# Kernel optimization log

Measured on AMD Instinct MI355X. Metric: run time of the kernel, lower is better.

The kernel has to match this reference:

```python
import jax, jax.numpy as jnp
import numpy as np

BETA = 0.25      # commitment loss weight
DECAY = 0.99     # EMA decay
EPS = 1e-5       # Laplace smoothing for counts


def setup_inputs() -> dict:
    key = jax.random.key(0)
    k1, k2, k3 = jax.random.split(key, 3)
    B, d, h, w, K = 16, 64, 64, 64, 1024
    z_e = jax.random.normal(k1, (B, d, h, w), dtype=jnp.float32)
    codebook = jax.random.normal(k2, (K, d), dtype=jnp.float32)
    ema_count = jnp.ones((K,), dtype=jnp.float32)
    ema_sum = jax.random.normal(k3, (K, d), dtype=jnp.float32)
    return {"z_e": z_e, "codebook": codebook, "ema_count": ema_count, "ema_sum": ema_sum}


def reference(z_e, codebook, ema_count, ema_sum):
    B, d, h, w = z_e.shape
    K = codebook.shape[0]
    # [B,d,h,w] -> [N,d], N = B*h*w
    z_flat = jnp.transpose(z_e, (0, 2, 3, 1)).reshape(-1, d)
    # squared euclidean distances [N,K]
    dist = (jnp.sum(z_flat * z_flat, axis=1, keepdims=True)
            - 2.0 * (z_flat @ codebook.T)
            + jnp.sum(codebook * codebook, axis=1)[None, :])
    indices = jnp.argmin(dist, axis=1)                      # [N] int
    e_k = codebook[indices].reshape(B, h, w, d).transpose(0, 3, 1, 2)  # [B,d,h,w]

    # --- EMA codebook update (training mode, no grad) ---
    zf = jax.lax.stop_gradient(z_flat)
    counts = jax.ops.segment_sum(jnp.ones((zf.shape[0],), dtype=zf.dtype), indices, num_segments=K)
    sums = jax.ops.segment_sum(zf, indices, num_segments=K)
    new_count = ema_count * DECAY + (1.0 - DECAY) * counts
    new_sum = ema_sum * DECAY + (1.0 - DECAY) * sums
    n = jnp.sum(new_count)
    count_s = (new_count + EPS) / (n + K * EPS) * n
    new_codebook = new_sum / count_s[:, None]

    # straight-through estimator
    e_k_ste = z_e + jax.lax.stop_gradient(e_k - z_e)
    L_commit = (jnp.mean((z_e - jax.lax.stop_gradient(e_k)) ** 2)
                + BETA * jnp.mean((jax.lax.stop_gradient(z_e) - e_k) ** 2))
    return (e_k_ste, indices.reshape(B, h, w), L_commit, new_codebook, new_count, new_sum)
```

## Files before the change

kernel.cpp:

```cpp
#include <hip/hip_runtime.h>
#include <hip/hip_bf16.h>
#include <hip/hip_fp16.h>

#define NB 16
#define DD 64
#define HW 4096
#define NTOT 65536
#define KC 1024

#define O_EK   0
#define O_IDX  4194304
#define O_L    4259840
#define O_CB   4259841
#define O_CNT  4325377
#define O_SUM  4326401

#define WS_IDX    0
#define WS_LCPART 65536
#define WS_N      66048
#define WS_CNORM  66560
#define WS_PSUM   67584
#define WS_PCNT   329728
#define WS_CBH    399360
#define WS_CBL    432128

typedef _Float16 v8h __attribute__((ext_vector_type(8)));
typedef float    v4f __attribute__((ext_vector_type(4)));
typedef unsigned short ush;

__global__ __launch_bounds__(256) void k_pre(const float* __restrict__ cb,
                                             const float* __restrict__ ema_count,
                                             float* __restrict__ cnorm,
                                             float* __restrict__ n_ws,
                                             unsigned short* __restrict__ cbh,
                                             unsigned short* __restrict__ cbl) {
    const int t = threadIdx.x;
    const int w = (blockIdx.x * 256 + t) >> 6;
    const int l = t & 63;
    float s = 0.f;
    if (l < 16) {
        float4 v = *(const float4*)(cb + (size_t)w * DD + l * 4);
        s = v.x * v.x + v.y * v.y + v.z * v.z + v.w * v.w;
    }
#pragma unroll
    for (int m = 1; m <= 8; m <<= 1) s += __shfl_xor(s, m, 64);
    if (l == 0) cnorm[w] = s;

    const int e4 = blockIdx.x * 256 + t;
    if (e4 < 16384) {
        float4 v4 = ((const float4*)cb)[e4];
        float sx = -2.f * v4.x, sy = -2.f * v4.y, sz = -2.f * v4.z, sw = -2.f * v4.w;
        __half hx = __float2half(sx), hy = __float2half(sy),
               hz = __float2half(sz), hw2 = __float2half(sw);
        ushort4 h4 = { __half_as_ushort(hx), __half_as_ushort(hy),
                       __half_as_ushort(hz), __half_as_ushort(hw2) };
        ((ushort4*)cbh)[e4] = h4;
        ushort4 l4 = { __half_as_ushort(__float2half(sx - __half2float(hx))),
                       __half_as_ushort(__float2half(sy - __half2float(hy))),
                       __half_as_ushort(__float2half(sz - __half2float(hz))),
                       __half_as_ushort(__float2half(sw - __half2float(hw2))) };
        ((ushort4*)cbl)[e4] = l4;
    }

    if (blockIdx.x == 0) {
        __shared__ float red[256];
        red[t] = ema_count[t] + ema_count[t + 256] + ema_count[t + 512] + ema_count[t + 768];
        __syncthreads();
        for (int s2 = 128; s2 >= 1; s2 >>= 1) {
            if (t < s2) red[t] += red[t + s2];
            __syncthreads();
        }
        if (t == 0) n_ws[0] = 0.99f * red[0] + 0.01f * 65536.0f;
    }
}

__global__ __launch_bounds__(512, 3) void k_argmin(const float* __restrict__ z_e,
                                                   const float* __restrict__ cbf,
                                                   const unsigned short* __restrict__ cbh,
                                                   const unsigned short* __restrict__ cbl,
                                                   const float* __restrict__ cnorm,
                                                   unsigned short* __restrict__ idx16,
                                                   float* __restrict__ out) {
    __shared__ __align__(16) unsigned char ldsAB[32768];
    __shared__ __align__(16) float slab[2048];
    __shared__ int idx_lds[128];
    __shared__ int flagrows[128];
    __shared__ int flagi1[128];
    __shared__ int flagi2[128];
    __shared__ int nflag;

    ush (*A2h)[128][8]  = (ush(*)[128][8])(ldsAB);
    ush (*A2l)[128][8]  = (ush(*)[128][8])(ldsAB + 16384);
    ush (*B2h)[8][64][8] = (ush(*)[8][64][8])(ldsAB);
    ush (*B2l)[8][64][8] = (ush(*)[8][64][8])(ldsAB + 16384);

    const int t  = threadIdx.x;
    const int n0 = blockIdx.x * 128;
    const int bb  = n0 >> 12;
    const int hw0 = n0 & 4095;
    const float* zbase = z_e + (size_t)bb * (DD * HW) + hw0;

    if (t == 0) nflag = 0;

    {
        const int jr   = t >> 5;
        const int m4   = (t & 31) << 2;
        const int chl  = t >> 8;
        const int cm   = t & 127;
        const int half = (t >> 7) & 1;
        for (int sl = 0; sl < 4; ++sl) {
            if (sl) __syncthreads();
            float4 v = *(const float4*)(zbase + (size_t)(sl * 16 + jr) * HW + m4);
            *(float4*)&slab[jr * 128 + m4] = v;
            __syncthreads();
            unsigned hv[2], lv[2];
#pragma unroll
            for (int p = 0; p < 2; ++p) {
                int jj = chl * 8 + half * 4 + p * 2;
                float v0 = slab[jj * 128 + cm];
                float v1 = slab[(jj + 1) * 128 + cm];
                __half h0 = __float2half(v0), h1 = __float2half(v1);
                __half l0 = __float2half(v0 - __half2float(h0));
                __half l1 = __float2half(v1 - __half2float(h1));
                hv[p] = (unsigned)__half_as_ushort(h0) | ((unsigned)__half_as_ushort(h1) << 16);
                lv[p] = (unsigned)__half_as_ushort(l0) | ((unsigned)__half_as_ushort(l1) << 16);
            }
            uint2 hq = {hv[0], hv[1]}, lq = {lv[0], lv[1]};
            *(uint2*)&A2h[sl * 2 + chl][cm][half * 4] = hq;
            *(uint2*)&A2l[sl * 2 + chl][cm][half * 4] = lq;
        }
    }
    __syncthreads();

    const int w    = t >> 6;
    const int lane = t & 63;
    const int c    = lane & 15;
    const int q    = lane >> 4;

    v8h Afh[2], Afl[2];
    {
        int m = 16 * w + c;
#pragma unroll
        for (int s = 0; s < 2; ++s) {
            Afh[s] = *(const v8h*)&A2h[s * 4 + q][m][0];
            Afl[s] = *(const v8h*)&A2l[s * 4 + q][m][0];
        }
    }
    __syncthreads();

    const int ch0   = t >> 6;
    const int code0 = t & 63;

    {
        size_t g0 = ((size_t)code0) * 64 + ch0 * 8;
        *(uint4*)&B2h[0][ch0][code0][0] = *(const uint4*)(cbh + g0);
        *(uint4*)&B2l[0][ch0][code0][0] = *(const uint4*)(cbl + g0);
    }
    __syncthreads();

    float m1f[4], m2f[4];
#pragma unroll
    for (int r = 0; r < 4; ++r) { m1f[r] = 3.4e38f; m2f[r] = 3.4e38f; }

    for (int kt = 0; kt < 16; ++kt) {
        const int cur = kt & 1, nxt = cur ^ 1;
        uint4 ph0, pl0;
        if (kt < 15) {
            size_t g0 = ((size_t)((kt + 1) * 64 + code0)) * 64 + ch0 * 8;
            ph0 = *(const uint4*)(cbh + g0);
            pl0 = *(const uint4*)(cbl + g0);
        }

#pragma unroll
        for (int sub = 0; sub < 4; ++sub) {
            const int cl = sub * 16 + c;
            v8h Bfh0 = *(const v8h*)&B2h[cur][q][cl][0];
            v8h Bfh1 = *(const v8h*)&B2h[cur][4 + q][cl][0];
            v8h Bfl0 = *(const v8h*)&B2l[cur][q][cl][0];
            v8h Bfl1 = *(const v8h*)&B2l[cur][4 + q][cl][0];
            const unsigned kg = (unsigned)(kt * 64 + cl);
            const float cnc = cnorm[kg];
            v4f acc = {cnc, cnc, cnc, cnc};
            acc = __builtin_amdgcn_mfma_f32_16x16x32_f16(Afh[0], Bfh0, acc, 0, 0, 0);
            acc = __builtin_amdgcn_mfma_f32_16x16x32_f16(Afh[1], Bfh1, acc, 0, 0, 0);
            acc = __builtin_amdgcn_mfma_f32_16x16x32_f16(Afh[0], Bfl0, acc, 0, 0, 0);
            acc = __builtin_amdgcn_mfma_f32_16x16x32_f16(Afh[1], Bfl1, acc, 0, 0, 0);
            acc = __builtin_amdgcn_mfma_f32_16x16x32_f16(Afl[0], Bfh0, acc, 0, 0, 0);
            acc = __builtin_amdgcn_mfma_f32_16x16x32_f16(Afl[1], Bfh1, acc, 0, 0, 0);
#pragma unroll
            for (int r = 0; r < 4; ++r) {
                unsigned vu = (__float_as_uint(acc[r]) & 0xFFFFFC00u) | kg;
                float vp = __uint_as_float(vu);
                m2f[r] = __builtin_amdgcn_fmed3f(m1f[r], m2f[r], vp);
                m1f[r] = fminf(m1f[r], vp);
            }
        }

        if (kt < 15) {
            *(uint4*)&B2h[nxt][ch0][code0][0] = ph0;
            *(uint4*)&B2l[nxt][ch0][code0][0] = pl0;
        }
        __syncthreads();
    }

#pragma unroll
    for (int r = 0; r < 4; ++r) {
        float a = m1f[r], b2 = m2f[r];
#pragma unroll
        for (int mask = 1; mask <= 8; mask <<= 1) {
            float o1 = __shfl_xor(a, mask, 64);
            float o2 = __shfl_xor(b2, mask, 64);
            float mx = fmaxf(a, o1);
            a  = fminf(a, o1);
            b2 = fminf(fminf(b2, o2), mx);
        }
        if (c == 0) {
            int row = 16 * w + q * 4 + r;
            int i1 = (int)(__float_as_uint(a) & 1023u);
            idx_lds[row] = i1;
            float margin = fmaf(fabsf(a), 6e-4f, 0.0015f);
            if (b2 - a < margin) {
                int p = atomicAdd(&nflag, 1);
                flagrows[p] = row;
                flagi1[p] = i1;
                flagi2[p] = (int)(__float_as_uint(b2) & 1023u);
            }
        }
    }
    __syncthreads();

    {
        int nf = nflag;
        for (int f = w; f < nf; f += 8) {
            int row = flagrows[f], i1 = flagi1[f], i2x = flagi2[f];
            const float* zrow = zbase + row;
            float zj = zrow[(size_t)lane * HW];
            float p1 = zj * cbf[(size_t)i1  * DD + lane];
            float p2 = zj * cbf[(size_t)i2x * DD + lane];
#pragma unroll
            for (int mask = 1; mask <= 32; mask <<= 1) {
                p1 += __shfl_xor(p1, mask, 64);
                p2 += __shfl_xor(p2, mask, 64);
            }
            if (lane == 0) {
                float d1 = fmaf(-2.0f, p1, cnorm[i1]);
                float d2 = fmaf(-2.0f, p2, cnorm[i2x]);
                if (d2 < d1 || (d2 == d1 && i2x < i1)) idx_lds[row] = i2x;
            }
        }
    }
    __syncthreads();

    if (t < 128) {
        int bi = idx_lds[t];
        out[O_IDX + n0 + t] = (float)bi;
        idx16[n0 + t] = (unsigned short)bi;
    }
}

__global__ __launch_bounds__(1024) void k_out(const unsigned short* __restrict__ idx16,
                                              const float* __restrict__ z_e,
                                              const float* __restrict__ cb,
                                              float* __restrict__ psum,
                                              int* __restrict__ pcnt,
                                              float* __restrict__ lc_part,
                                              float* __restrict__ out) {
    __shared__ float acc[KC];
    __shared__ int bins[KC];
    __shared__ float cbj[KC];
    __shared__ float lcr[16];
    const int j = blockIdx.x & 63;
    const int c = blockIdx.x >> 6;
    const int t = threadIdx.x;
    acc[t] = 0.f;
    bins[t] = 0;
    cbj[t] = cb[(size_t)t * DD + j];
    __syncthreads();
    const float* zj = z_e + (size_t)j * HW;
    float* oj = out + O_EK + (size_t)j * HW;
    const int base = c * 16384;
    float lc = 0.f;
#pragma unroll
    for (int i = 0; i < 4; ++i) {
        int n4 = base + i * 4096 + t * 4;
        int b = n4 >> 12, hw = n4 & 4095;
        size_t zoff = (size_t)b * (DD * HW) + hw;
        float4 z4 = *(const float4*)(zj + zoff);
        ushort4 k4 = *(const ushort4*)(idx16 + n4);
        float e0 = cbj[k4.x], e1 = cbj[k4.y], e2 = cbj[k4.z], e3 = cbj[k4.w];
        float4 o4 = { z4.x + (e0 - z4.x), z4.y + (e1 - z4.y),
                      z4.z + (e2 - z4.z), z4.w + (e3 - z4.w) };
        *(float4*)(oj + zoff) = o4;
        float d0 = z4.x - e0, d1 = z4.y - e1, d2 = z4.z - e2, d3 = z4.w - e3;
        lc = fmaf(d0, d0, lc); lc = fmaf(d1, d1, lc);
        lc = fmaf(d2, d2, lc); lc = fmaf(d3, d3, lc);
        atomicAdd(&acc[k4.x], z4.x);
        atomicAdd(&acc[k4.y], z4.y);
        atomicAdd(&acc[k4.z], z4.z);
        atomicAdd(&acc[k4.w], z4.w);
        if (j == 0) {
            atomicAdd(&bins[k4.x], 1); atomicAdd(&bins[k4.y], 1);
            atomicAdd(&bins[k4.z], 1); atomicAdd(&bins[k4.w], 1);
        }
    }
    __syncthreads();
    psum[(size_t)c * 65536 + j * 1024 + t] = acc[t];
    if (j == 0) pcnt[c * 1024 + t] = bins[t];
#pragma unroll
    for (int m = 32; m >= 1; m >>= 1) lc += __shfl_xor(lc, m, 64);
    if ((t & 63) == 0) lcr[t >> 6] = lc;
    __syncthreads();
    if (t == 0) {
        float s = 0.f;
#pragma unroll
        for (int u = 0; u < 16; ++u) s += lcr[u];
        lc_part[blockIdx.x] = s;
    }
}

__global__ __launch_bounds__(1024) void k_epi(const float* __restrict__ psum,
                                              const int* __restrict__ pcnt,
                                              const float* __restrict__ ema_sum,
                                              const float* __restrict__ ema_count,
                                              const float* __restrict__ n_ws,
                                              const float* __restrict__ lc_part,
                                              float* __restrict__ out) {
    const int t = threadIdx.x;
    const int e = blockIdx.x * 1024 + t;
    const int k = e >> 6, j = e & 63;
    float s4 = psum[j * 1024 + k] + psum[65536 + j * 1024 + k]
             + psum[131072 + j * 1024 + k] + psum[196608 + j * 1024 + k];
    float ns = ema_sum[e] * 0.99f + 0.01f * s4;
    out[O_SUM + e] = ns;
    int cnt = pcnt[k] + pcnt[1024 + k] + pcnt[2048 + k] + pcnt[3072 + k];
    float nc = ema_count[k] * 0.99f + 0.01f * (float)cnt;
    float n  = n_ws[0];
    float cs = (nc + 1e-5f) / (n + 1024.0f * 1e-5f) * n;
    out[O_CB + e] = ns / cs;
    if (blockIdx.x == 0) {
        int c2 = pcnt[t] + pcnt[1024 + t] + pcnt[2048 + t] + pcnt[3072 + t];
        out[O_CNT + t] = ema_count[t] * 0.99f + 0.01f * (float)c2;
    }
    if (blockIdx.x == 1) {
        __shared__ float red[512];
        if (t < 512) red[t] = (t < 256) ? lc_part[t] : 0.f;
        __syncthreads();
        for (int s = 256; s >= 1; s >>= 1) {
            if (t < s) red[t] += red[t + s];
            __syncthreads();
        }
        if (t == 0) out[O_L] = 1.25f * red[0] * (1.0f / 4194304.0f);
    }
}

extern "C" void kernel_launch(void* const* d_in, const int* in_sizes, int n_in,
                              void* d_out, int out_size, void* d_ws, size_t ws_size,
                              hipStream_t stream) {
    const float* z_e       = (const float*)d_in[0];
    const float* cb        = (const float*)d_in[1];
    const float* ema_count = (const float*)d_in[2];
    const float* ema_sum   = (const float*)d_in[3];
    float* out             = (float*)d_out;

    float* ws_f      = (float*)d_ws;
    unsigned short* idx16 = (unsigned short*)d_ws;
    float* lc_part   = ws_f + WS_LCPART;
    float* n_ws      = ws_f + WS_N;
    float* cnorm_ws  = ws_f + WS_CNORM;
    float* psum      = ws_f + WS_PSUM;
    int*   pcnt      = (int*)(ws_f + WS_PCNT);
    unsigned short* cbh = (unsigned short*)(ws_f + WS_CBH);
    unsigned short* cbl = (unsigned short*)(ws_f + WS_CBL);

    k_pre<<<256, 256, 0, stream>>>(cb, ema_count, cnorm_ws, n_ws, cbh, cbl);
    k_argmin<<<NTOT / 128, 512, 0, stream>>>(z_e, cb, cbh, cbl, cnorm_ws, idx16, out);
    k_out<<<256, 1024, 0, stream>>>(idx16, z_e, cb, psum, pcnt, lc_part, out);
    k_epi<<<64, 1024, 0, stream>>>(psum, pcnt, ema_sum, ema_count, n_ws, lc_part, out);
}
```

Measured before the change: 137.8 us.

## Split codebook across two wave groups with 2x row tiles per wave

The argmin kernel now splits its 8 waves into two streams, each scanning half the codebook tiles. Each wave covers 32 rows instead of 16, so every B fragment read from LDS feeds twice as many MFMAs. The per-stream min/second-min pairs are merged through shared memory before flagging ambiguous rows. LDS grows to 64KB for per-stream double buffers and launch bounds rise to 4 blocks per CU, which adds register pressure and may cap occupancy.

```diff
diff --git a/kernel.cpp b/kernel.cpp
--- a/kernel.cpp
+++ b/kernel.cpp
@@ -74,15 +74,15 @@
     }
 }
 
-__global__ __launch_bounds__(512, 3) void k_argmin(const float* __restrict__ z_e,
+__global__ __launch_bounds__(512, 4) void k_argmin(const float* __restrict__ z_e,
                                                    const float* __restrict__ cbf,
                                                    const unsigned short* __restrict__ cbh,
                                                    const unsigned short* __restrict__ cbl,
                                                    const float* __restrict__ cnorm,
                                                    unsigned short* __restrict__ idx16,
                                                    float* __restrict__ out) {
-    __shared__ __align__(16) unsigned char ldsAB[32768];
-    __shared__ __align__(16) float slab[2048];
+    __shared__ __align__(16) unsigned char ldsAB[65536];
+    __shared__ float2 mm[2][128];
     __shared__ int idx_lds[128];
     __shared__ int flagrows[128];
     __shared__ int flagi1[128];
@@ -91,8 +91,9 @@
 
     ush (*A2h)[128][8]  = (ush(*)[128][8])(ldsAB);
     ush (*A2l)[128][8]  = (ush(*)[128][8])(ldsAB + 16384);
-    ush (*B2h)[8][64][8] = (ush(*)[8][64][8])(ldsAB);
-    ush (*B2l)[8][64][8] = (ush(*)[8][64][8])(ldsAB + 16384);
+    float* slab = (float*)(ldsAB + 32768);
+    ush (*B2h)[2][8][64][8] = (ush(*)[2][8][64][8])(ldsAB);
+    ush (*B2l)[2][8][64][8] = (ush(*)[2][8][64][8])(ldsAB + 32768);
 
     const int t  = threadIdx.x;
     const int n0 = blockIdx.x * 128;
@@ -133,98 +134,128 @@
     __syncthreads();
 
     const int w    = t >> 6;
+    const int strm = w >> 2;
+    const int wl   = w & 3;
     const int lane = t & 63;
     const int c    = lane & 15;
     const int q    = lane >> 4;
 
-    v8h Afh[2], Afl[2];
-    {
-        int m = 16 * w + c;
+    v8h Afh[2][2], Afl[2][2];
+#pragma unroll
+    for (int g = 0; g < 2; ++g) {
+        int m = 32 * wl + 16 * g + c;
 #pragma unroll
         for (int s = 0; s < 2; ++s) {
-            Afh[s] = *(const v8h*)&A2h[s * 4 + q][m][0];
-            Afl[s] = *(const v8h*)&A2l[s * 4 + q][m][0];
-        }
-    }
-    __syncthreads();
-
-    const int ch0   = t >> 6;
-    const int code0 = t & 63;
-
-    {
-        size_t g0 = ((size_t)code0) * 64 + ch0 * 8;
-        *(uint4*)&B2h[0][ch0][code0][0] = *(const uint4*)(cbh + g0);
-        *(uint4*)&B2l[0][ch0][code0][0] = *(const uint4*)(cbl + g0);
-    }
-    __syncthreads();
-
-    float m1f[4], m2f[4];
-#pragma unroll
-    for (int r = 0; r < 4; ++r) { m1f[r] = 3.4e38f; m2f[r] = 3.4e38f; }
-
-    for (int kt = 0; kt < 16; ++kt) {
-        const int cur = kt & 1, nxt = cur ^ 1;
-        uint4 ph0, pl0;
-        if (kt < 15) {
-            size_t g0 = ((size_t)((kt + 1) * 64 + code0)) * 64 + ch0 * 8;
-            ph0 = *(const uint4*)(cbh + g0);
-            pl0 = *(const uint4*)(cbl + g0);
+            Afh[g][s] = *(const v8h*)&A2h[s * 4 + q][m][0];
+            Afl[g][s] = *(const v8h*)&A2l[s * 4 + q][m][0];
+        }
+    }
+    __syncthreads();
+
+    const int tid   = t & 255;
+    const int scode = tid & 63;
+    const int sch   = tid >> 6;
+    const int ktb   = strm * 8;
+
+#pragma unroll
+    for (int i = 0; i < 2; ++i) {
+        int ch = sch + 4 * i;
+        size_t g0 = ((size_t)(ktb * 64 + scode)) * 64 + ch * 8;
+        *(uint4*)&B2h[strm][0][ch][scode][0] = *(const uint4*)(cbh + g0);
+        *(uint4*)&B2l[strm][0][ch][scode][0] = *(const uint4*)(cbl + g0);
+    }
+    __syncthreads();
+
+    float m1f[2][4], m2f[2][4];
+#pragma unroll
+    for (int g = 0; g < 2; ++g)
+#pragma unroll
+        for (int r = 0; r < 4; ++r) { m1f[g][r] = 3.4e38f; m2f[g][r] = 3.4e38f; }
+
+    for (int it = 0; it < 8; ++it) {
+        const int cur = it & 1, nxt = cur ^ 1;
+        uint4 ph[2], pl[2];
+        if (it < 7) {
+#pragma unroll
+            for (int i = 0; i < 2; ++i) {
+                int ch = sch + 4 * i;
+                size_t g0 = ((size_t)((ktb + it + 1) * 64 + scode)) * 64 + ch * 8;
+                ph[i] = *(const uint4*)(cbh + g0);
+                pl[i] = *(const uint4*)(cbl + g0);
+            }
         }
 
 #pragma unroll
         for (int sub = 0; sub < 4; ++sub) {
             const int cl = sub * 16 + c;
-            v8h Bfh0 = *(const v8h*)&B2h[cur][q][cl][0];
-            v8h Bfh1 = *(const v8h*)&B2h[cur][4 + q][cl][0];
-            v8h Bfl0 = *(const v8h*)&B2l[cur][q][cl][0];
-            v8h Bfl1 = *(const v8h*)&B2l[cur][4 + q][cl][0];
-            const unsigned kg = (unsigned)(kt * 64 + cl);
+            v8h Bfh0 = *(const v8h*)&B2h[strm][cur][q][cl][0];
+            v8h Bfh1 = *(const v8h*)&B2h[strm][cur][4 + q][cl][0];
+            v8h Bfl0 = *(const v8h*)&B2l[strm][cur][q][cl][0];
+            v8h Bfl1 = *(const v8h*)&B2l[strm][cur][4 + q][cl][0];
+            const unsigned kg = (unsigned)((ktb + it) * 64 + cl);
             const float cnc = cnorm[kg];
-            v4f acc = {cnc, cnc, cnc, cnc};
-            acc = __builtin_amdgcn_mfma_f32_16x16x32_f16(Afh[0], Bfh0, acc, 0, 0, 0);
-            acc = __builtin_amdgcn_mfma_f32_16x16x32_f16(Afh[1], Bfh1, acc, 0, 0, 0);
-            acc = __builtin_amdgcn_mfma_f32_16x16x32_f16(Afh[0], Bfl0, acc, 0, 0, 0);
-            acc = __builtin_amdgcn_mfma_f32_16x16x32_f16(Afh[1], Bfl1, acc, 0, 0, 0);
-            acc = __builtin_amdgcn_mfma_f32_16x16x32_f16(Afl[0], Bfh0, acc, 0, 0, 0);
-            acc = __builtin_amdgcn_mfma_f32_16x16x32_f16(Afl[1], Bfh1, acc, 0, 0, 0);
-#pragma unroll
-            for (int r = 0; r < 4; ++r) {
-                unsigned vu = (__float_as_uint(acc[r]) & 0xFFFFFC00u) | kg;
-                float vp = __uint_as_float(vu);
-                m2f[r] = __builtin_amdgcn_fmed3f(m1f[r], m2f[r], vp);
-                m1f[r] = fminf(m1f[r], vp);
-            }
-        }
-
-        if (kt < 15) {
-            *(uint4*)&B2h[nxt][ch0][code0][0] = ph0;
-            *(uint4*)&B2l[nxt][ch0][code0][0] = pl0;
+#pragma unroll
+            for (int g = 0; g < 2; ++g) {
+                v4f acc = {cnc, cnc, cnc, cnc};
+                acc = __builtin_amdgcn_mfma_f32_16x16x32_f16(Afh[g][0], Bfh0, acc, 0, 0, 0);
+                acc = __builtin_amdgcn_mfma_f32_16x16x32_f16(Afh[g][1], Bfh1, acc, 0, 0, 0);
+                acc = __builtin_amdgcn_mfma_f32_16x16x32_f16(Afh[g][0], Bfl0, acc, 0, 0, 0);
+                acc = __builtin_amdgcn_mfma_f32_16x16x32_f16(Afh[g][1], Bfl1, acc, 0, 0, 0);
+                acc = __builtin_amdgcn_mfma_f32_16x16x32_f16(Afl[g][0], Bfh0, acc, 0, 0, 0);
+                acc = __builtin_amdgcn_mfma_f32_16x16x32_f16(Afl[g][1], Bfh1, acc, 0, 0, 0);
+#pragma unroll
+                for (int r = 0; r < 4; ++r) {
+                    unsigned vu = (__float_as_uint(acc[r]) & 0xFFFFFC00u) | kg;
+                    float vp = __uint_as_float(vu);
+                    m2f[g][r] = __builtin_amdgcn_fmed3f(m1f[g][r], m2f[g][r], vp);
+                    m1f[g][r] = fminf(m1f[g][r], vp);
+                }
+            }
+        }
+
+        if (it < 7) {
+#pragma unroll
+            for (int i = 0; i < 2; ++i) {
+                int ch = sch + 4 * i;
+                *(uint4*)&B2h[strm][nxt][ch][scode][0] = ph[i];
+                *(uint4*)&B2l[strm][nxt][ch][scode][0] = pl[i];
+            }
         }
         __syncthreads();
     }
 
 #pragma unroll
-    for (int r = 0; r < 4; ++r) {
-        float a = m1f[r], b2 = m2f[r];
-#pragma unroll
-        for (int mask = 1; mask <= 8; mask <<= 1) {
-            float o1 = __shfl_xor(a, mask, 64);
-            float o2 = __shfl_xor(b2, mask, 64);
-            float mx = fmaxf(a, o1);
-            a  = fminf(a, o1);
-            b2 = fminf(fminf(b2, o2), mx);
-        }
-        if (c == 0) {
-            int row = 16 * w + q * 4 + r;
-            int i1 = (int)(__float_as_uint(a) & 1023u);
-            idx_lds[row] = i1;
-            float margin = fmaf(fabsf(a), 6e-4f, 0.0015f);
-            if (b2 - a < margin) {
-                int p = atomicAdd(&nflag, 1);
-                flagrows[p] = row;
-                flagi1[p] = i1;
-                flagi2[p] = (int)(__float_as_uint(b2) & 1023u);
-            }
+    for (int g = 0; g < 2; ++g)
+#pragma unroll
+        for (int r = 0; r < 4; ++r) {
+            float a = m1f[g][r], b2 = m2f[g][r];
+#pragma unroll
+            for (int mask = 1; mask <= 8; mask <<= 1) {
+                float o1 = __shfl_xor(a, mask, 64);
+                float o2 = __shfl_xor(b2, mask, 64);
+                float mx = fmaxf(a, o1);
+                a  = fminf(a, o1);
+                b2 = fminf(fminf(b2, o2), mx);
+            }
+            if (c == 0) {
+                int row = 32 * wl + 16 * g + q * 4 + r;
+                mm[strm][row] = make_float2(a, b2);
+            }
+        }
+    __syncthreads();
+
+    if (t < 128) {
+        float2 A = mm[0][t], B = mm[1][t];
+        float a  = fminf(A.x, B.x);
+        float b2 = fminf(fminf(A.y, B.y), fmaxf(A.x, B.x));
+        int i1 = (int)(__float_as_uint(a) & 1023u);
+        idx_lds[t] = i1;
+        float margin = fmaf(fabsf(a), 6e-4f, 0.0015f);
+        if (b2 - a < margin) {
+            int p = atomicAdd(&nflag, 1);
+            flagrows[p] = t;
+            flagi1[p] = i1;
+            flagi2[p] = (int)(__float_as_uint(b2) & 1023u);
         }
     }
     __syncthreads();
```

Result: no change. 139.4 us (+1.2%).
